# Kernel tuning notes

Measured on AMD Instinct MI355X. Metric: run time of the kernel, lower is better.

## Reference

```python
import math
import jax, jax.numpy as jnp
import numpy as np

B, L, D, H = 2, 2048, 1024, 16
HD = D // H  # 64

def setup_inputs() -> dict:
    key = jax.random.key(0)
    k1, k2, k3 = jax.random.split(key, 3)
    x = jax.random.normal(k1, (B, L, D), dtype=jnp.float32)
    Wqkv = jax.random.normal(k2, (3 * D, D), dtype=jnp.float32) * (1.0 / math.sqrt(D))
    Wo = jax.random.normal(k3, (D, D), dtype=jnp.float32) * (1.0 / math.sqrt(D))
    return {"x": x, "Wqkv": Wqkv, "Wo": Wo}

def reference(x, Wqkv, Wo):
    # QKV projection (torch Linear: y = x @ W.T), then split
    qkv = jnp.einsum('bld,ed->ble', x, Wqkv)  # [B, L, 3D]
    q, k, v = jnp.split(qkv, 3, axis=-1)
    # [B, H, L, HD]
    q = q.reshape(B, L, H, HD).transpose(0, 2, 1, 3)
    k = k.reshape(B, L, H, HD).transpose(0, 2, 1, 3)
    v = v.reshape(B, L, H, HD).transpose(0, 2, 1, 3)
    # scores; causal mask applied before the 1/sqrt(d) scale (as in source;
    # -inf is unchanged by scaling so math matches scale-then-mask)
    scores = jnp.einsum('bhqd,bhkd->bhqk', q, k)
    causal = jnp.tril(jnp.ones((L, L), dtype=bool))
    scores = jnp.where(causal, scores, -jnp.inf)
    attn = jax.nn.softmax(scores / math.sqrt(HD), axis=-1)
    out = jnp.einsum('bhqk,bhkd->bhqd', attn, v)  # [B, H, L, HD]
    out = out.transpose(0, 2, 1, 3).reshape(B, L, D)
    # output projection (dropout is identity in eval / p=0)
    return jnp.einsum('bld,ed->ble', out, Wo)
```

## Files before the change

### kernel.cpp

```cpp
#include <hip/hip_runtime.h>
#include <hip/hip_bf16.h>
#include <cstdint>
#include <cstddef>

#define B_SZ 2
#define L_SEQ 2048
#define DM 1024
#define NH 16
#define HDIM 64
#define BL (B_SZ * L_SEQ)
#define QKV_N (3 * DM)

typedef __attribute__((ext_vector_type(4))) float f32x4;
typedef __attribute__((ext_vector_type(16))) float f32x16;
typedef __attribute__((ext_vector_type(8))) short bf16x8;
typedef __attribute__((ext_vector_type(2))) unsigned int u32x2;
typedef __attribute__((ext_vector_type(4))) unsigned int u32x4;
typedef unsigned short u16;
typedef __attribute__((ext_vector_type(4))) unsigned short u16x4;

__device__ __forceinline__ float bf2f(u16 u) {
  union { unsigned int i; float f; } c; c.i = ((unsigned int)u) << 16; return c.f;
}
__device__ __forceinline__ u16 f2bf(float f) {
  union { float f; unsigned int i; } c; c.f = f;
  unsigned int r = c.i + 0x7fffu + ((c.i >> 16) & 1u);
  return (u16)(r >> 16);
}

__device__ __forceinline__ void gload_lds16(const void* g, void* l) {
  __builtin_amdgcn_global_load_lds(
      (const __attribute__((address_space(1))) void*)g,
      (__attribute__((address_space(3))) void*)l, 16, 0, 0);
}

__device__ __forceinline__ f32x16 mfma32(bf16x8 a, bf16x8 b, f32x16 c) {
  return __builtin_amdgcn_mfma_f32_32x32x16_bf16(a, b, c, 0, 0, 0);
}

__device__ __forceinline__ unsigned cvtpk(float lo, float hi) {
  unsigned r;
  asm("v_cvt_pk_bf16_f32 %0, %1, %2" : "=v"(r) : "v"(lo), "v"(hi));
  return r;
}
__device__ __forceinline__ void plswap(unsigned& a, unsigned& b) {
  asm("v_permlane32_swap_b32 %0, %1" : "+v"(a), "+v"(b));
}

template <int BASE>
__device__ __forceinline__ bf16x8 pack_bfrag(const f32x16& v) {
  unsigned a  = cvtpk(v[BASE + 0], v[BASE + 1]);
  unsigned a2 = cvtpk(v[BASE + 2], v[BASE + 3]);
  unsigned b  = cvtpk(v[BASE + 4], v[BASE + 5]);
  unsigned b2 = cvtpk(v[BASE + 6], v[BASE + 7]);
  plswap(a, b);
  plswap(a2, b2);
  u32x4 fw; fw[0] = a; fw[1] = a2; fw[2] = b; fw[3] = b2;
  return __builtin_bit_cast(bf16x8, fw);
}

#define N4_X  (BL * DM / 4)
#define N4_WQ (QKV_N * DM / 4)
#define N4_WO (DM * DM / 4)
__global__ __launch_bounds__(256) void cvt_all(
    const float* __restrict__ x, const float* __restrict__ wqkv,
    const float* __restrict__ wo, u16* __restrict__ x_bf,
    u16* __restrict__ w_bf, u16* __restrict__ wo_bf) {
  int i = blockIdx.x * blockDim.x + threadIdx.x;
  const int stride = gridDim.x * blockDim.x;
  const int total = N4_X + N4_WQ + N4_WO;
  for (; i < total; i += stride) {
    const float4* src;
    u16x4* dst;
    if (i < N4_X) {
      src = (const float4*)x + i; dst = (u16x4*)x_bf + i;
    } else if (i < N4_X + N4_WQ) {
      src = (const float4*)wqkv + (i - N4_X); dst = (u16x4*)w_bf + (i - N4_X);
    } else {
      src = (const float4*)wo + (i - N4_X - N4_WQ);
      dst = (u16x4*)wo_bf + (i - N4_X - N4_WQ);
    }
    float4 v = *src;
    u16x4 o;
    o[0] = f2bf(v.x); o[1] = f2bf(v.y); o[2] = f2bf(v.z); o[3] = f2bf(v.w);
    *dst = o;
  }
}

template <bool BF16_OUT>
__global__ __launch_bounds__(256) void gemm_bt(
    const u16* __restrict__ A, const u16* __restrict__ B,
    void* __restrict__ Cv, int M, int N, int K) {
  __shared__ u16 As[128 * 64];
  __shared__ u16 Bs[128 * 64];
  const int tid = threadIdx.x;
  const int lane = tid & 63, w = tid >> 6;
  const int lr = lane & 15, lg = lane >> 4;
  const int wr = w >> 1, wc = w & 1;
  const int bm = blockIdx.y * 128, bn = blockIdx.x * 128;

  f32x4 acc[4][4] = {};

  const int srow = lane >> 3;
  const int csw = ((lane & 7) ^ srow) * 8;
  const size_t abase = (size_t)(bm + w * 32 + srow) * K + csw;
  const size_t bbase = (size_t)(bn + w * 32 + srow) * K + csw;
  const int sw_rd = lr & 7;

  for (int k0 = 0; k0 < K; k0 += 64) {
#pragma unroll
    for (int c = 0; c < 4; ++c)
      gload_lds16(A + abase + (size_t)c * 8 * K + k0, &As[(w * 32 + c * 8) * 64]);
#pragma unroll
    for (int c = 0; c < 4; ++c)
      gload_lds16(B + bbase + (size_t)c * 8 * K + k0, &Bs[(w * 32 + c * 8) * 64]);
    __syncthreads();

#pragma unroll
    for (int kk = 0; kk < 2; ++kk) {
      bf16x8 af[4], bfr[4];
#pragma unroll
      for (int mt = 0; mt < 4; ++mt) {
        const int row = wr * 64 + mt * 16 + lr;
        af[mt] = *(const bf16x8*)&As[row * 64 + (((kk * 4 + lg) ^ sw_rd) * 8)];
      }
#pragma unroll
      for (int nt = 0; nt < 4; ++nt) {
        const int row = wc * 64 + nt * 16 + lr;
        bfr[nt] = *(const bf16x8*)&Bs[row * 64 + (((kk * 4 + lg) ^ sw_rd) * 8)];
      }
#pragma unroll
      for (int mt = 0; mt < 4; ++mt)
#pragma unroll
        for (int nt = 0; nt < 4; ++nt)
          acc[mt][nt] = __builtin_amdgcn_mfma_f32_16x16x32_bf16(
              af[mt], bfr[nt], acc[mt][nt], 0, 0, 0);
    }
    __syncthreads();
  }

#pragma unroll
  for (int mt = 0; mt < 4; ++mt)
#pragma unroll
    for (int nt = 0; nt < 4; ++nt)
#pragma unroll
      for (int r = 0; r < 4; ++r) {
        const int row = bm + wr * 64 + mt * 16 + lg * 4 + r;
        const int col = bn + wc * 64 + nt * 16 + lr;
        if (BF16_OUT)
          ((u16*)Cv)[(size_t)row * N + col] = f2bf(acc[mt][nt][r]);
        else
          ((float*)Cv)[(size_t)row * N + col] = acc[mt][nt][r];
      }
}

__device__ const uint8_t JST[20] = {7,7,7,7, 6,6,6, 5,5,5, 4,4, 3,3, 2, 1,
                                    6, 4, 2, 0};
__device__ const uint8_t JT0[20] = {0,8,16,24, 0,8,16, 0,8,16, 0,8, 0,8, 0, 0,
                                    24, 16, 8, 0};
__device__ const uint8_t JT1[20] = {8,16,24,32, 8,16,24, 8,16,24, 8,16, 8,16, 8, 8,
                                    28, 20, 12, 4};
__device__ const uint8_t SB[8]   = {255, 255, 0, 2, 4, 7, 10, 14};
__device__ const uint8_t SCNT[8] = {1, 1, 2, 2, 3, 3, 4, 4};

__global__ __launch_bounds__(512) void attn_fused(const u16* __restrict__ qkv,
                                                  u16* __restrict__ aout,
                                                  u16* __restrict__ opart_lo,
                                                  u16* __restrict__ opart_hi,
                                                  float* __restrict__ lpart) {
  __shared__ u16 Kl[2][64 * 64];
  __shared__ u16 Vt[2][64 * 64];

  const int tid = threadIdx.x;
  const int lane = tid & 63, w = tid >> 6;
  const int l31 = lane & 31, hi = lane >> 5;
  const int id = (int)blockIdx.x;
  const int bh = id & 31, j = id >> 5;
  const int st = JST[j];
  const int t0 = JT0[j], t1 = JT1[j];
  const int b = bh >> 4, h = bh & 15;
  const u16* base = qkv + (size_t)b * L_SEQ * QKV_N;
  const int W = st * 256 + w * 32;
  const int qrow = W + l31;

  const int krow = tid >> 3;
  const int ks = tid & 7;
  const int kr7 = krow & 7;
  const u16* gpk_base = base + (size_t)krow * QKV_N + DM + h * HDIM + ks * 8;
  bf16x8 kr;

  const int vd0 = (tid & 31) * 2;
  const int vkg = tid >> 5;
  const int vge = tid & 7;
  const int vgo = (tid & 7) ^ 4;
  const u16* gpv_base = base + (size_t)(vkg * 4) * QKV_N + 2 * DM + h * HDIM + vd0;
  unsigned int vtmp[4];

  auto issue_loads = [&](int t) {
    kr = *(const bf16x8*)(gpk_base + (size_t)t * 64 * QKV_N);
    const u16* gpv = gpv_base + (size_t)t * 64 * QKV_N;
#pragma unroll
    for (int jj = 0; jj < 4; ++jj)
      vtmp[jj] = *(const unsigned int*)(gpv + (size_t)jj * QKV_N);
  };
  auto write_lds = [&](int buf) {
    *(bf16x8*)&Kl[buf][krow * 64 + ((ks ^ kr7) * 8)] = kr;
    u32x2 lo, hiw;
    lo[0]  = __builtin_amdgcn_perm(vtmp[1], vtmp[0], 0x05040100u);
    lo[1]  = __builtin_amdgcn_perm(vtmp[3], vtmp[2], 0x05040100u);
    hiw[0] = __builtin_amdgcn_perm(vtmp[1], vtmp[0], 0x07060302u);
    hiw[1] = __builtin_amdgcn_perm(vtmp[3], vtmp[2], 0x07060302u);
    *(u32x2*)&Vt[buf][vd0 * 64 + (((vkg >> 1) ^ vge) * 8) + (vkg & 1) * 4] = lo;
    *(u32x2*)&Vt[buf][(vd0 + 1) * 64 + (((vkg >> 1) ^ vgo) * 8) + (vkg & 1) * 4] = hiw;
  };

  bf16x8 bq[4];
  {
    const u16* qp = base + (size_t)qrow * QKV_N + h * HDIM + hi * 8;
#pragma unroll
    for (int dc = 0; dc < 4; ++dc) {
      bf16x8 tq = *(const bf16x8*)(qp + dc * 16);
#pragma unroll
      for (int i = 0; i < 8; ++i)
        tq[i] = (short)f2bf(bf2f((u16)tq[i]) * 0.18033688f);
      bq[dc] = tq;
    }
  }

  f32x16 acc0 = {}, acc1 = {};
  float lrow = 0.f;

  const int vg = ((l31 >> 1) & 7) ^ ((l31 & 1) << 2);
  const int lsw = l31 & 7;

  issue_loads(t0);
  write_lds(0);
  __syncthreads();

  for (int t = t0; t < t1; ++t) {
    const int cur = (t - t0) & 1;
    if (t + 1 < t1) issue_loads(t + 1);

    if (64 * t <= W + 31) {
      f32x16 s0 = {}, s1 = {};
#pragma unroll
      for (int dc = 0; dc < 4; ++dc) {
        const int sl = ((dc * 2 + hi) ^ lsw) * 8;
        const bf16x8 k0 = *(const bf16x8*)&Kl[cur][l31 * 64 + sl];
        const bf16x8 k1 = *(const bf16x8*)&Kl[cur][(32 + l31) * 64 + sl];
        s0 = mfma32(k0, bq[dc], s0);
        s1 = mfma32(k1, bq[dc], s1);
      }

      if (64 * t + 63 > W) {
#pragma unroll
        for (int r = 0; r < 16; ++r) {
          const int kg = t * 64 + (r & 3) + 8 * (r >> 2) + 4 * hi;
          if (kg > qrow) s0[r] = -1e30f;
          if (kg + 32 > qrow) s1[r] = -1e30f;
        }
      }

#pragma unroll
      for (int r = 0; r < 16; ++r) {
        s0[r] = exp2f(s0[r]);
        s1[r] = exp2f(s1[r]);
      }
      float r0 = 0.f, r1 = 0.f, r2 = 0.f, r3 = 0.f;
#pragma unroll
      for (int r = 0; r < 16; r += 4) {
        r0 += s0[r] + s0[r + 1];
        r1 += s0[r + 2] + s0[r + 3];
        r2 += s1[r] + s1[r + 1];
        r3 += s1[r + 2] + s1[r + 3];
      }
      lrow += (r0 + r1) + (r2 + r3);

      const bf16x8 pf0 = pack_bfrag<0>(s0);
      const bf16x8 pf1 = pack_bfrag<8>(s0);
      const bf16x8 pf2 = pack_bfrag<0>(s1);
      const bf16x8 pf3 = pack_bfrag<8>(s1);

#pragma unroll
      for (int c = 0; c < 4; ++c) {
        const bf16x8 pf = c == 0 ? pf0 : c == 1 ? pf1 : c == 2 ? pf2 : pf3;
        const int sl = ((c * 2 + hi) ^ vg) * 8;
        const bf16x8 va = *(const bf16x8*)&Vt[cur][l31 * 64 + sl];
        const bf16x8 vb = *(const bf16x8*)&Vt[cur][(32 + l31) * 64 + sl];
        acc0 = mfma32(va, pf, acc0);
        acc1 = mfma32(vb, pf, acc1);
      }
    }

    if (t + 1 < t1) write_lds(((t + 1) - t0) & 1);
    __syncthreads();
  }

  lrow += __shfl_xor(lrow, 32);

  if (SB[st] != 255) {
    const int c = t0 >> 3;
    const int slot = ((int)SB[st] + c) * 32 + bh;
    u16* po = slot < 512 ? opart_lo + (size_t)slot * 16384
                         : opart_hi + (size_t)(slot - 512) * 16384;
    const int q = w * 32 + l31;
#pragma unroll
    for (int i = 0; i < 16; ++i) {
      const int d0 = (i & 3) + 8 * (i >> 2) + 4 * hi;
      po[d0 * 256 + q] = f2bf(acc0[i]);
      po[(d0 + 32) * 256 + q] = f2bf(acc1[i]);
    }
    if (hi == 0) lpart[slot * 256 + q] = lrow;
  } else {
    const float inv = 1.f / lrow;
#pragma unroll
    for (int i = 0; i < 16; ++i) { acc0[i] *= inv; acc1[i] *= inv; }
    const bf16x8 of0 = pack_bfrag<0>(acc0);
    const bf16x8 of1 = pack_bfrag<8>(acc0);
    const bf16x8 of2 = pack_bfrag<0>(acc1);
    const bf16x8 of3 = pack_bfrag<8>(acc1);
    u16* op = aout + (size_t)(b * L_SEQ + qrow) * DM + h * HDIM + hi * 8;
    *(bf16x8*)(op + 0)  = of0;
    *(bf16x8*)(op + 16) = of1;
    *(bf16x8*)(op + 32) = of2;
    *(bf16x8*)(op + 48) = of3;
  }
}

__global__ __launch_bounds__(256) void attn_combine(
    const u16* __restrict__ opart_lo, const u16* __restrict__ opart_hi,
    const float* __restrict__ lpart, u16* __restrict__ aout) {
  const int gid = (int)blockIdx.x * 256 + (int)threadIdx.x;
  const int q = gid & 255;
  const int u = gid >> 8;
  const int st = 2 + (u >> 5), bh = u & 31;
  const int b = bh >> 4, h = bh & 15;
  const int nc = (int)SCNT[st];
  const int sb = (int)SB[st];

  const u16* pp[4];
  float L = 0.f;
#pragma unroll
  for (int c = 0; c < 4; ++c)
    if (c < nc) {
      const int slot = (sb + c) * 32 + bh;
      L += lpart[slot * 256 + q];
      pp[c] = slot < 512 ? opart_lo + (size_t)slot * 16384
                         : opart_hi + (size_t)(slot - 512) * 16384;
    }
  const float invl = 1.f / L;

  const int qrow = st * 256 + q;
  u16* op = aout + (size_t)(b * L_SEQ + qrow) * DM + h * HDIM;
#pragma unroll
  for (int d0 = 0; d0 < 64; d0 += 8) {
    float v[8] = {};
#pragma unroll
    for (int c = 0; c < 4; ++c)
      if (c < nc) {
#pragma unroll
        for (int jj = 0; jj < 8; ++jj)
          v[jj] += bf2f(pp[c][(d0 + jj) * 256 + q]);
      }
    u16x4 oa, ob;
#pragma unroll
    for (int jj = 0; jj < 4; ++jj) {
      oa[jj] = f2bf(v[jj] * invl);
      ob[jj] = f2bf(v[jj + 4] * invl);
    }
    *(u16x4*)(op + d0) = oa;
    *(u16x4*)(op + d0 + 4) = ob;
  }
}

extern "C" void kernel_launch(void* const* d_in, const int* in_sizes, int n_in,
                              void* d_out, int out_size, void* d_ws, size_t ws_size,
                              hipStream_t stream) {
  (void)in_sizes; (void)n_in; (void)out_size; (void)ws_size;
  const float* x = (const float*)d_in[0];
  const float* wqkv = (const float*)d_in[1];
  const float* wo = (const float*)d_in[2];

  char* ws = (char*)d_ws;
  u16* x_bf = (u16*)(ws);
  u16* w_bf = (u16*)(ws + (size_t)(8u << 20));
  u16* wo_bf = (u16*)(ws + (size_t)(14u << 20));
  u16* qkv_bf = (u16*)(ws + (size_t)(16u << 20));
  u16* ao_bf = x_bf;
  u16* opart_lo = (u16*)d_out;
  u16* opart_hi = (u16*)(ws + (size_t)(8u << 20));
  float* lpart = (float*)(ws + (size_t)(10u << 20));

  cvt_all<<<2048, 256, 0, stream>>>(x, wqkv, wo, x_bf, w_bf, wo_bf);

  dim3 g1(QKV_N / 128, BL / 128);
  gemm_bt<true><<<g1, 256, 0, stream>>>(x_bf, w_bf, (void*)qkv_bf, BL, QKV_N, DM);

  attn_fused<<<dim3(640), 512, 0, stream>>>(qkv_bf, ao_bf, opart_lo, opart_hi, lpart);
  attn_combine<<<dim3(192), 256, 0, stream>>>(opart_lo, opart_hi, lpart, ao_bf);

  dim3 g3(DM / 128, BL / 128);
  gemm_bt<false><<<g3, 256, 0, stream>>>(ao_bf, wo_bf, d_out, BL, DM, DM);
}
```

Baseline: 129.2 us.

## Switch GEMM to 32x32x16 MFMA tiles and XCD-aware block swizzle

```diff
diff --git a/kernel.cpp b/kernel.cpp
--- a/kernel.cpp
+++ b/kernel.cpp
@@ -90,22 +90,25 @@
 template <bool BF16_OUT>
 __global__ __launch_bounds__(256) void gemm_bt(
     const u16* __restrict__ A, const u16* __restrict__ B,
-    void* __restrict__ Cv, int M, int N, int K) {
+    void* __restrict__ Cv, int M, int N, int K, int nbx) {
   __shared__ u16 As[128 * 64];
   __shared__ u16 Bs[128 * 64];
   const int tid = threadIdx.x;
   const int lane = tid & 63, w = tid >> 6;
-  const int lr = lane & 15, lg = lane >> 4;
+  const int l31 = lane & 31, hi = lane >> 5;
   const int wr = w >> 1, wc = w & 1;
-  const int bm = blockIdx.y * 128, bn = blockIdx.x * 128;
-
-  f32x4 acc[4][4] = {};
+
+  const int bid = (int)blockIdx.x;
+  const int swz = (bid & 7) * ((int)gridDim.x >> 3) + (bid >> 3);
+  const int bm = (swz / nbx) * 128, bn = (swz % nbx) * 128;
+
+  f32x16 acc00 = {}, acc01 = {}, acc10 = {}, acc11 = {};
 
   const int srow = lane >> 3;
   const int csw = ((lane & 7) ^ srow) * 8;
   const size_t abase = (size_t)(bm + w * 32 + srow) * K + csw;
   const size_t bbase = (size_t)(bn + w * 32 + srow) * K + csw;
-  const int sw_rd = lr & 7;
+  const int sw = l31 & 7;
 
   for (int k0 = 0; k0 < K; k0 += 64) {
 #pragma unroll
@@ -117,41 +120,37 @@
     __syncthreads();
 
 #pragma unroll
-    for (int kk = 0; kk < 2; ++kk) {
-      bf16x8 af[4], bfr[4];
-#pragma unroll
-      for (int mt = 0; mt < 4; ++mt) {
-        const int row = wr * 64 + mt * 16 + lr;
-        af[mt] = *(const bf16x8*)&As[row * 64 + (((kk * 4 + lg) ^ sw_rd) * 8)];
-      }
-#pragma unroll
-      for (int nt = 0; nt < 4; ++nt) {
-        const int row = wc * 64 + nt * 16 + lr;
-        bfr[nt] = *(const bf16x8*)&Bs[row * 64 + (((kk * 4 + lg) ^ sw_rd) * 8)];
-      }
-#pragma unroll
-      for (int mt = 0; mt < 4; ++mt)
-#pragma unroll
-        for (int nt = 0; nt < 4; ++nt)
-          acc[mt][nt] = __builtin_amdgcn_mfma_f32_16x16x32_bf16(
-              af[mt], bfr[nt], acc[mt][nt], 0, 0, 0);
+    for (int ks = 0; ks < 4; ++ks) {
+      const int sl = ((ks * 2 + hi) ^ sw) * 8;
+      const bf16x8 a0 = *(const bf16x8*)&As[(wr * 64 + l31) * 64 + sl];
+      const bf16x8 a1 = *(const bf16x8*)&As[(wr * 64 + 32 + l31) * 64 + sl];
+      const bf16x8 b0 = *(const bf16x8*)&Bs[(wc * 64 + l31) * 64 + sl];
+      const bf16x8 b1 = *(const bf16x8*)&Bs[(wc * 64 + 32 + l31) * 64 + sl];
+      acc00 = mfma32(a0, b0, acc00);
+      acc01 = mfma32(a0, b1, acc01);
+      acc10 = mfma32(a1, b0, acc10);
+      acc11 = mfma32(a1, b1, acc11);
     }
     __syncthreads();
   }
 
-#pragma unroll
-  for (int mt = 0; mt < 4; ++mt)
-#pragma unroll
-    for (int nt = 0; nt < 4; ++nt)
-#pragma unroll
-      for (int r = 0; r < 4; ++r) {
-        const int row = bm + wr * 64 + mt * 16 + lg * 4 + r;
-        const int col = bn + wc * 64 + nt * 16 + lr;
-        if (BF16_OUT)
-          ((u16*)Cv)[(size_t)row * N + col] = f2bf(acc[mt][nt][r]);
-        else
-          ((float*)Cv)[(size_t)row * N + col] = acc[mt][nt][r];
-      }
+#define CWRITE(ACC, MI, NI)                                                    \
+  {                                                                            \
+    _Pragma("unroll")                                                          \
+    for (int r = 0; r < 16; ++r) {                                             \
+      const int row = bm + wr * 64 + (MI)*32 + (r & 3) + 8 * (r >> 2) + 4 * hi;\
+      const int col = bn + wc * 64 + (NI)*32 + l31;                            \
+      if (BF16_OUT)                                                            \
+        ((u16*)Cv)[(size_t)row * N + col] = f2bf(ACC[r]);                      \
+      else                                                                     \
+        ((float*)Cv)[(size_t)row * N + col] = ACC[r];                          \
+    }                                                                          \
+  }
+  CWRITE(acc00, 0, 0)
+  CWRITE(acc01, 0, 1)
+  CWRITE(acc10, 1, 0)
+  CWRITE(acc11, 1, 1)
+#undef CWRITE
 }
 
 __device__ const uint8_t JST[20] = {7,7,7,7, 6,6,6, 5,5,5, 4,4, 3,3, 2, 1,
@@ -393,12 +392,12 @@
 
   cvt_all<<<2048, 256, 0, stream>>>(x, wqkv, wo, x_bf, w_bf, wo_bf);
 
-  dim3 g1(QKV_N / 128, BL / 128);
-  gemm_bt<true><<<g1, 256, 0, stream>>>(x_bf, w_bf, (void*)qkv_bf, BL, QKV_N, DM);
+  gemm_bt<true><<<dim3(768), 256, 0, stream>>>(x_bf, w_bf, (void*)qkv_bf,
+                                               BL, QKV_N, DM, QKV_N / 128);
 
   attn_fused<<<dim3(640), 512, 0, stream>>>(qkv_bf, ao_bf, opart_lo, opart_hi, lpart);
   attn_combine<<<dim3(192), 256, 0, stream>>>(opart_lo, opart_hi, lpart, ao_bf);
 
-  dim3 g3(DM / 128, BL / 128);
-  gemm_bt<false><<<g3, 256, 0, stream>>>(ao_bf, wo_bf, d_out, BL, DM, DM);
-}
+  gemm_bt<false><<<dim3(256), 256, 0, stream>>>(ao_bf, wo_bf, d_out,
+                                                BL, DM, DM, DM / 128);
+}
```

Measured after the change: 124.3 us. 3.8% less time.
